# Performance work log

Measured on AMD Instinct MI355X. Metric: run time of the kernel, lower is better.

## Reference

```python
import jax, jax.numpy as jnp
import numpy as np

B, S, D, H = 4, 2048, 1024, 16
HD = D // H  # head dim = 64


def setup_inputs() -> dict:
    key = jax.random.key(0)
    ks = jax.random.split(key, 6)
    hidden_states = jax.random.normal(ks[0], (B, S, D), dtype=jnp.float32)
    attention_mask = jnp.zeros((B, S), dtype=bool)  # ignored by the module (set to None in forward)
    # RoPE cache: standard rotary angles per position
    inv_freq = 1.0 / (10000.0 ** (jnp.arange(0, HD, 2, dtype=jnp.float32) / HD))  # [HD/2]
    ang = jnp.arange(S, dtype=jnp.float32)[:, None] * inv_freq[None, :]  # [S, HD/2]
    ang = jnp.concatenate([ang, ang], axis=-1)  # [S, HD]
    rope_cos = jnp.cos(ang)
    rope_sin = jnp.sin(ang)
    scale = 1.0 / np.sqrt(D)
    Wq = jax.random.normal(ks[1], (D, D), dtype=jnp.float32) * scale
    Wk = jax.random.normal(ks[2], (D, D), dtype=jnp.float32) * scale
    Wv = jax.random.normal(ks[3], (D, D), dtype=jnp.float32) * scale
    return {"hidden_states": hidden_states, "attention_mask": attention_mask,
            "rope_cos": rope_cos, "rope_sin": rope_sin, "Wq": Wq, "Wk": Wk, "Wv": Wv}


def _rotate_half(x):
    x1, x2 = jnp.split(x, 2, axis=-1)
    return jnp.concatenate([-x2, x1], axis=-1)


def _apply_rope(x, cos, sin):
    # x: [B, H, S, HD]; cos/sin: [S, HD]
    return x * cos[None, None, :, :] + _rotate_half(x) * sin[None, None, :, :]


def reference(hidden_states, attention_mask, rope_cos, rope_sin, Wq, Wk, Wv):
    del attention_mask  # forward() sets attention_mask = None
    b, s, d = hidden_states.shape
    # QKV projections (nn.Linear: y = x @ W.T), split into heads -> [B, H, S, HD]
    def proj(W):
        y = jnp.einsum('bsd,ed->bse', hidden_states, W)
        return y.reshape(b, s, H, HD).transpose(0, 2, 1, 3)
    q = _apply_rope(proj(Wq), rope_cos, rope_sin)
    k = _apply_rope(proj(Wk), rope_cos, rope_sin)
    v = proj(Wv)
    # Softmax attention (non-causal, dropout_p=0)
    scores = jnp.einsum('bhqd,bhkd->bhqk', q, k) / np.sqrt(HD)
    probs = jax.nn.softmax(scores, axis=-1)
    ctx = jnp.einsum('bhqk,bhkd->bhqd', probs, v)
    # [B, H, S, HD] -> [B, S, D]
    return ctx.transpose(0, 2, 1, 3).reshape(b, s, d)
```

## Files before the change

### kernel.cpp

```cpp
#include <hip/hip_runtime.h>
#include <hip/hip_bf16.h>
#include <stdint.h>


typedef __attribute__((ext_vector_type(4))) float    f32x4;
typedef __attribute__((ext_vector_type(8))) __bf16   bf16x8;
typedef __attribute__((ext_vector_type(8))) unsigned short ushort8;
typedef __attribute__((ext_vector_type(4))) unsigned short ushort4v;

#define QSCALE 0.18033688011112042f
#define SMAX   16.0f

#define GLOAD_LDS16(g, l)                                                     \
  __builtin_amdgcn_global_load_lds(                                           \
      (const __attribute__((address_space(1))) void*)(g),                     \
      (__attribute__((address_space(3))) void*)(l), 16, 0, 0)

__device__ inline unsigned short bf(float f) {
  return __builtin_bit_cast(unsigned short, (__bf16)f);
}

__global__ __launch_bounds__(256) void cvt_bf16(
    const float* __restrict__ X,
    const float* __restrict__ Wq, const float* __restrict__ Wk,
    const float* __restrict__ Wv,
    unsigned short* __restrict__ Xb, unsigned short* __restrict__ Wb)
{
  const int seg = blockIdx.y;
  const float* __restrict__ src = (seg == 0) ? X : (seg == 1) ? Wq : (seg == 2) ? Wk : Wv;
  unsigned short* __restrict__ dst = (seg == 0) ? Xb : Wb + (size_t)(seg - 1) * 1048576;
  const size_t n8 = (seg == 0) ? (size_t)1048576 : (size_t)131072;
  const size_t stride = (size_t)gridDim.x * 256;
  for (size_t i = blockIdx.x * 256 + threadIdx.x; i < n8; i += stride) {
    const float4 a = *reinterpret_cast<const float4*>(src + i * 8);
    const float4 b = *reinterpret_cast<const float4*>(src + i * 8 + 4);
    ushort8 o = { bf(a.x), bf(a.y), bf(a.z), bf(a.w), bf(b.x), bf(b.y), bf(b.z), bf(b.w) };
    *reinterpret_cast<ushort8*>(dst + i * 8) = o;
  }
}

__global__ __launch_bounds__(256) void qkv_gemm(
    const unsigned short* __restrict__ Xb, const unsigned short* __restrict__ Wb,
    const float* __restrict__ rc, const float* __restrict__ rs,
    unsigned short* __restrict__ Qb, unsigned short* __restrict__ Kb,
    unsigned short* __restrict__ VbT, int col0, int nheads_c, int gx)
{
  const int nwg = gridDim.x;
  const int q8 = nwg >> 3;
  int w = (blockIdx.x % 8) * q8 + blockIdx.x / 8;
  const int z = w / (gx * 64);
  const int r = w - z * gx * 64;
  const int brow = (r / gx) * 128;
  const int bcol = (r % gx) * 128;

  const unsigned short* __restrict__ Wz = Wb + (size_t)z * 1048576;
  const bool rope = (z < 2);

  const int tid  = threadIdx.x;
  const int lane = tid & 63;
  const int wid  = tid >> 6;
  const int wm = wid >> 1, wn = wid & 1;
  const int col16 = lane & 15, rowg = lane >> 4;

  __shared__ unsigned short As[128 * 32];
  __shared__ unsigned short Bs[128 * 32];

  f32x4 acc[4][4];
  #pragma unroll
  for (int m = 0; m < 4; ++m)
    #pragma unroll
    for (int n = 0; n < 4; ++n) acc[m][n] = (f32x4)0.f;

  const int srow = wid * 16 + (lane >> 2);
  const int scol = (lane & 3) * 8;
  const unsigned short* gA0 = Xb + (size_t)(brow + srow) * 1024 + scol;
  const unsigned short* gA1 = gA0 + (size_t)64 * 1024;
  const unsigned short* gB0 = Wz + (size_t)(col0 + bcol + srow) * 1024 + scol;
  const unsigned short* gB1 = gB0 + (size_t)64 * 1024;
  unsigned short* lA0 = &As[wid * 16 * 32];
  unsigned short* lA1 = &As[(64 + wid * 16) * 32];
  unsigned short* lB0 = &Bs[wid * 16 * 32];
  unsigned short* lB1 = &Bs[(64 + wid * 16) * 32];

  for (int k0 = 0; k0 < 1024; k0 += 32) {
    GLOAD_LDS16(gA0 + k0, lA0);
    GLOAD_LDS16(gA1 + k0, lA1);
    GLOAD_LDS16(gB0 + k0, lB0);
    GLOAD_LDS16(gB1 + k0, lB1);
    __syncthreads();

    bf16x8 af[4], bfv[4];
    #pragma unroll
    for (int m = 0; m < 4; ++m)
      af[m] = __builtin_bit_cast(bf16x8, *reinterpret_cast<const ushort8*>(
                &As[(wm * 64 + m * 16 + col16) * 32 + rowg * 8]));
    #pragma unroll
    for (int n = 0; n < 4; ++n)
      bfv[n] = __builtin_bit_cast(bf16x8, *reinterpret_cast<const ushort8*>(
                &Bs[(wn * 64 + n * 16 + col16) * 32 + rowg * 8]));
    #pragma unroll
    for (int m = 0; m < 4; ++m)
      #pragma unroll
      for (int n = 0; n < 4; ++n)
        acc[m][n] = __builtin_amdgcn_mfma_f32_16x16x32_bf16(af[m], bfv[n], acc[m][n], 0, 0, 0);
    __syncthreads();
  }

  #pragma unroll
  for (int m = 0; m < 4; ++m) {
    #pragma unroll
    for (int n = 0; n < 4; ++n) {
      const int e  = bcol + wn * 64 + n * 16 + col16;
      const int hl = e >> 6, hd = e & 63;
      if (z == 2) {
        const int row0 = brow + wm * 64 + m * 16 + rowg * 4;
        const int b = row0 >> 11, s0 = row0 & 2047;
        ushort4v o = { bf(acc[m][n][0]), bf(acc[m][n][1]), bf(acc[m][n][2]), bf(acc[m][n][3]) };
        *reinterpret_cast<ushort4v*>(
            VbT + ((size_t)(b * nheads_c + hl) * 64 + hd) * 2048 + s0) = o;
      } else {
        unsigned short* __restrict__ outp = (z == 0) ? Qb : Kb;
        #pragma unroll
        for (int j = 0; j < 4; ++j) {
          const int row = brow + wm * 64 + m * 16 + rowg * 4 + j;
          const int b = row >> 11, s = row & 2047;
          const float rot = (n < 2) ? -acc[m][n + 2][j] : acc[m][n - 2][j];
          float v = acc[m][n][j] * rc[s * 64 + hd] + rot * rs[s * 64 + hd];
          if (z == 0) v *= QSCALE;
          outp[((size_t)(b * nheads_c + hl) * 2048 + s) * 64 + hd] = bf(v);
        }
      }
    }
  }
}

__global__ __launch_bounds__(256) void attn(
    const unsigned short* __restrict__ Qb, const unsigned short* __restrict__ Kb,
    const unsigned short* __restrict__ VbT, float* __restrict__ out,
    int col0, int nheads_c)
{
  const int tid = threadIdx.x, lane = tid & 63, wq = tid >> 6;
  const int col16 = lane & 15, rowg = lane >> 4;

  int wg = blockIdx.x;
  const int qx = (int)gridDim.x >> 3;
  wg = (wg & 7) * qx + (wg >> 3);
  const int bh = wg >> 4;
  const int q0 = (wg & 15) * 128;
  const int b = bh / nheads_c, hl = bh - b * nheads_c;
  const int hg = (col0 >> 6) + hl;
  const size_t base = (size_t)bh * 2048 * 64;

  __shared__ unsigned short Ks[64 * 72];
  __shared__ unsigned short Vt[64 * 72];
  __shared__ unsigned short Ps[128 * 76];

  {
    const int r = tid >> 3, c = (tid & 7) * 8;
    #pragma unroll
    for (int p = 0; p < 4; ++p) {
      const int row = p * 32 + r;
      ushort8 v = *reinterpret_cast<const ushort8*>(Qb + base + (size_t)(q0 + row) * 64 + c);
      *reinterpret_cast<ushort8*>(&Ps[row * 76 + c]) = v;
    }
  }
  __syncthreads();
  bf16x8 qf[2][2];
  #pragma unroll
  for (int m = 0; m < 2; ++m)
    #pragma unroll
    for (int ks = 0; ks < 2; ++ks)
      qf[m][ks] = __builtin_bit_cast(bf16x8, *reinterpret_cast<const ushort8*>(
          &Ps[(wq * 32 + m * 16 + col16) * 76 + ks * 32 + rowg * 8]));

  float lsum[2][4];
  f32x4 acc[2][4];
  #pragma unroll
  for (int m = 0; m < 2; ++m)
    #pragma unroll
    for (int j = 0; j < 4; ++j) lsum[m][j] = 0.f;
  #pragma unroll
  for (int m = 0; m < 2; ++m)
    #pragma unroll
    for (int hf = 0; hf < 4; ++hf) acc[m][hf] = (f32x4)0.f;

  for (int kt = 0; kt < 32; ++kt) {
    const int key0 = kt * 64;
    {
      const int r = tid >> 3, c = (tid & 7) * 8;
      #pragma unroll
      for (int p = 0; p < 2; ++p) {
        ushort8 kv = *reinterpret_cast<const ushort8*>(Kb + base + (size_t)(key0 + p * 32 + r) * 64 + c);
        *reinterpret_cast<ushort8*>(&Ks[(p * 32 + r) * 72 + c]) = kv;
      }
      const int vr = tid >> 2, vc = (tid & 3) * 16;
      ushort8 v0 = *reinterpret_cast<const ushort8*>(VbT + base + (size_t)vr * 2048 + key0 + vc);
      ushort8 v1 = *reinterpret_cast<const ushort8*>(VbT + base + (size_t)vr * 2048 + key0 + vc + 8);
      *reinterpret_cast<ushort8*>(&Vt[vr * 72 + vc]) = v0;
      *reinterpret_cast<ushort8*>(&Vt[vr * 72 + vc + 8]) = v1;
    }
    __syncthreads();

    f32x4 sc[2][4];
    #pragma unroll
    for (int m = 0; m < 2; ++m)
      #pragma unroll
      for (int kf = 0; kf < 4; ++kf) sc[m][kf] = (f32x4)0.f;
    __builtin_amdgcn_s_setprio(1);
    #pragma unroll
    for (int kf = 0; kf < 4; ++kf) {
      #pragma unroll
      for (int ks = 0; ks < 2; ++ks) {
        bf16x8 kfrag = __builtin_bit_cast(bf16x8, *reinterpret_cast<const ushort8*>(
            &Ks[(kf * 16 + col16) * 72 + ks * 32 + rowg * 8]));
        sc[0][kf] = __builtin_amdgcn_mfma_f32_16x16x32_bf16(qf[0][ks], kfrag, sc[0][kf], 0, 0, 0);
        sc[1][kf] = __builtin_amdgcn_mfma_f32_16x16x32_bf16(qf[1][ks], kfrag, sc[1][kf], 0, 0, 0);
      }
    }
    __builtin_amdgcn_s_setprio(0);

    #pragma unroll
    for (int m = 0; m < 2; ++m)
      #pragma unroll
      for (int j = 0; j < 4; ++j) {
        float ps = 0.f;
        #pragma unroll
        for (int kf = 0; kf < 4; ++kf) {
          const float p = __builtin_exp2f(sc[m][kf][j] - SMAX);
          sc[m][kf][j] = p;
          ps += p;
        }
        lsum[m][j] += ps;
      }

    #pragma unroll
    for (int m = 0; m < 2; ++m)
      #pragma unroll
      for (int kf = 0; kf < 4; ++kf)
        #pragma unroll
        for (int j = 0; j < 4; ++j)
          Ps[(wq * 32 + m * 16 + rowg * 4 + j) * 76 + kf * 16 + col16] = bf(sc[m][kf][j]);
    __syncthreads();

    __builtin_amdgcn_s_setprio(1);
    #pragma unroll
    for (int ks = 0; ks < 2; ++ks) {
      bf16x8 pf[2];
      #pragma unroll
      for (int m = 0; m < 2; ++m)
        pf[m] = __builtin_bit_cast(bf16x8, *reinterpret_cast<const ushort8*>(
            &Ps[(wq * 32 + m * 16 + col16) * 76 + ks * 32 + rowg * 8]));
      #pragma unroll
      for (int hf = 0; hf < 4; ++hf) {
        bf16x8 vf = __builtin_bit_cast(bf16x8, *reinterpret_cast<const ushort8*>(
            &Vt[(hf * 16 + col16) * 72 + ks * 32 + rowg * 8]));
        acc[0][hf] = __builtin_amdgcn_mfma_f32_16x16x32_bf16(pf[0], vf, acc[0][hf], 0, 0, 0);
        acc[1][hf] = __builtin_amdgcn_mfma_f32_16x16x32_bf16(pf[1], vf, acc[1][hf], 0, 0, 0);
      }
    }
    __builtin_amdgcn_s_setprio(0);
    __syncthreads();
  }

  #pragma unroll
  for (int m = 0; m < 2; ++m)
    #pragma unroll
    for (int j = 0; j < 4; ++j) {
      float l = lsum[m][j];
      l += __shfl_xor(l, 1);
      l += __shfl_xor(l, 2);
      l += __shfl_xor(l, 4);
      l += __shfl_xor(l, 8);
      const float inv = 1.0f / l;
      const int s = q0 + wq * 32 + m * 16 + rowg * 4 + j;
      #pragma unroll
      for (int hf = 0; hf < 4; ++hf) {
        const int hd = hf * 16 + col16;
        out[((size_t)(b * 2048 + s)) * 1024 + hg * 64 + hd] = acc[m][hf][j] * inv;
      }
    }
}

extern "C" void kernel_launch(void* const* d_in, const int* in_sizes, int n_in,
                              void* d_out, int out_size, void* d_ws, size_t ws_size,
                              hipStream_t stream) {
  (void)in_sizes; (void)n_in; (void)out_size;
  const float* X  = (const float*)d_in[0];
  const float* rc = (const float*)d_in[2];
  const float* rs = (const float*)d_in[3];
  const float* Wq = (const float*)d_in[4];
  const float* Wk = (const float*)d_in[5];
  const float* Wv = (const float*)d_in[6];
  float* out = (float*)d_out;

  const size_t fixed = (size_t)2 * 8192 * 1024 + (size_t)3 * 2 * 1024 * 1024;
  int NC = 8;
  for (int nc = 1; nc <= 8; nc <<= 1) {
    size_t need = (size_t)3 * 2 * 8192 * (1024 / nc) + fixed;
    if (need <= ws_size) { NC = nc; break; }
  }
  const int CW = 1024 / NC;
  const int nheads_c = CW >> 6;
  const int nBH = 4 * nheads_c;
  const int gx = CW / 128;
  const size_t pc = (size_t)8192 * CW;

  unsigned short* Qb  = (unsigned short*)d_ws;
  unsigned short* Kb  = Qb + pc;
  unsigned short* VbT = Kb + pc;
  unsigned short* Xb  = VbT + pc;
  unsigned short* Wb  = Xb + (size_t)8192 * 1024;

  cvt_bf16<<<dim3(512, 4), 256, 0, stream>>>(X, Wq, Wk, Wv, Xb, Wb);

  for (int c = 0; c < NC; ++c) {
    const int col0 = c * CW;
    qkv_gemm<<<dim3(gx * 64 * 3), 256, 0, stream>>>(
        Xb, Wb, rc, rs, Qb, Kb, VbT, col0, nheads_c, gx);
    attn<<<dim3(16 * nBH), 256, 0, stream>>>(
        Qb, Kb, VbT, out, col0, nheads_c);
  }
}
```

Before: 206.0 us.

## Prefetch next K/V tile into registers during attention compute

The attention loop now issues the global loads for the next 64-key K and V tile into registers before computing the current tile. After the PV MFMAs those registers are written to LDS, so global latency overlaps with compute instead of stalling at the top of each iteration. The first tile is preloaded together with Q, and the s_setprio wave-priority hints are removed. It costs extra registers per thread, which may lower occupancy.

```diff
diff --git a/kernel.cpp b/kernel.cpp
--- a/kernel.cpp
+++ b/kernel.cpp
@@ -54,7 +54,6 @@
   const int bcol = (r % gx) * 128;
 
   const unsigned short* __restrict__ Wz = Wb + (size_t)z * 1048576;
-  const bool rope = (z < 2);
 
   const int tid  = threadIdx.x;
   const int lane = tid & 63;
@@ -155,16 +154,27 @@
   __shared__ unsigned short Vt[64 * 72];
   __shared__ unsigned short Ps[128 * 76];
 
+  const int r  = tid >> 3, c  = (tid & 7) * 8;
+  const int vr = tid >> 2, vc = (tid & 3) * 16;
+
+  #pragma unroll
+  for (int p = 0; p < 4; ++p) {
+    const int row = p * 32 + r;
+    ushort8 v = *reinterpret_cast<const ushort8*>(Qb + base + (size_t)(q0 + row) * 64 + c);
+    *reinterpret_cast<ushort8*>(&Ps[row * 76 + c]) = v;
+  }
   {
-    const int r = tid >> 3, c = (tid & 7) * 8;
-    #pragma unroll
-    for (int p = 0; p < 4; ++p) {
-      const int row = p * 32 + r;
-      ushort8 v = *reinterpret_cast<const ushort8*>(Qb + base + (size_t)(q0 + row) * 64 + c);
-      *reinterpret_cast<ushort8*>(&Ps[row * 76 + c]) = v;
-    }
+    ushort8 k0 = *reinterpret_cast<const ushort8*>(Kb + base + (size_t)r * 64 + c);
+    ushort8 k1 = *reinterpret_cast<const ushort8*>(Kb + base + (size_t)(32 + r) * 64 + c);
+    ushort8 v0 = *reinterpret_cast<const ushort8*>(VbT + base + (size_t)vr * 2048 + vc);
+    ushort8 v1 = *reinterpret_cast<const ushort8*>(VbT + base + (size_t)vr * 2048 + vc + 8);
+    *reinterpret_cast<ushort8*>(&Ks[r * 72 + c]) = k0;
+    *reinterpret_cast<ushort8*>(&Ks[(32 + r) * 72 + c]) = k1;
+    *reinterpret_cast<ushort8*>(&Vt[vr * 72 + vc]) = v0;
+    *reinterpret_cast<ushort8*>(&Vt[vr * 72 + vc + 8]) = v1;
   }
   __syncthreads();
+
   bf16x8 qf[2][2];
   #pragma unroll
   for (int m = 0; m < 2; ++m)
@@ -185,28 +195,20 @@
     for (int hf = 0; hf < 4; ++hf) acc[m][hf] = (f32x4)0.f;
 
   for (int kt = 0; kt < 32; ++kt) {
-    const int key0 = kt * 64;
-    {
-      const int r = tid >> 3, c = (tid & 7) * 8;
-      #pragma unroll
-      for (int p = 0; p < 2; ++p) {
-        ushort8 kv = *reinterpret_cast<const ushort8*>(Kb + base + (size_t)(key0 + p * 32 + r) * 64 + c);
-        *reinterpret_cast<ushort8*>(&Ks[(p * 32 + r) * 72 + c]) = kv;
-      }
-      const int vr = tid >> 2, vc = (tid & 3) * 16;
-      ushort8 v0 = *reinterpret_cast<const ushort8*>(VbT + base + (size_t)vr * 2048 + key0 + vc);
-      ushort8 v1 = *reinterpret_cast<const ushort8*>(VbT + base + (size_t)vr * 2048 + key0 + vc + 8);
-      *reinterpret_cast<ushort8*>(&Vt[vr * 72 + vc]) = v0;
-      *reinterpret_cast<ushort8*>(&Vt[vr * 72 + vc + 8]) = v1;
-    }
-    __syncthreads();
+    ushort8 nk0, nk1, nv0, nv1;
+    if (kt < 31) {
+      const int kn = (kt + 1) * 64;
+      nk0 = *reinterpret_cast<const ushort8*>(Kb + base + (size_t)(kn + r) * 64 + c);
+      nk1 = *reinterpret_cast<const ushort8*>(Kb + base + (size_t)(kn + 32 + r) * 64 + c);
+      nv0 = *reinterpret_cast<const ushort8*>(VbT + base + (size_t)vr * 2048 + kn + vc);
+      nv1 = *reinterpret_cast<const ushort8*>(VbT + base + (size_t)vr * 2048 + kn + vc + 8);
+    }
 
     f32x4 sc[2][4];
     #pragma unroll
     for (int m = 0; m < 2; ++m)
       #pragma unroll
       for (int kf = 0; kf < 4; ++kf) sc[m][kf] = (f32x4)0.f;
-    __builtin_amdgcn_s_setprio(1);
     #pragma unroll
     for (int kf = 0; kf < 4; ++kf) {
       #pragma unroll
@@ -217,7 +219,6 @@
         sc[1][kf] = __builtin_amdgcn_mfma_f32_16x16x32_bf16(qf[1][ks], kfrag, sc[1][kf], 0, 0, 0);
       }
     }
-    __builtin_amdgcn_s_setprio(0);
 
     #pragma unroll
     for (int m = 0; m < 2; ++m)
@@ -242,7 +243,6 @@
           Ps[(wq * 32 + m * 16 + rowg * 4 + j) * 76 + kf * 16 + col16] = bf(sc[m][kf][j]);
     __syncthreads();
 
-    __builtin_amdgcn_s_setprio(1);
     #pragma unroll
     for (int ks = 0; ks < 2; ++ks) {
       bf16x8 pf[2];
@@ -258,8 +258,15 @@
         acc[1][hf] = __builtin_amdgcn_mfma_f32_16x16x32_bf16(pf[1], vf, acc[1][hf], 0, 0, 0);
       }
     }
-    __builtin_amdgcn_s_setprio(0);
     __syncthreads();
+
+    if (kt < 31) {
+      *reinterpret_cast<ushort8*>(&Ks[r * 72 + c]) = nk0;
+      *reinterpret_cast<ushort8*>(&Ks[(32 + r) * 72 + c]) = nk1;
+      *reinterpret_cast<ushort8*>(&Vt[vr * 72 + vc]) = nv0;
+      *reinterpret_cast<ushort8*>(&Vt[vr * 72 + vc + 8]) = nv1;
+      __syncthreads();
+    }
   }
 
   #pragma unroll
```

After: 216.7 us. +5.2%, slower.

## Double-buffer K/V tiles via direct-to-LDS loads with XOR swizzle and MFMA row sums

Applied to the files above, without the earlier changes.

The attention kernel now prefetches the next K and V^T tiles straight into a second LDS buffer using global_load_lds, so global loads overlap the current tile's compute. Those tiles use an unpadded, XOR-swizzled layout to avoid bank conflicts. The softmax denominator is now computed by an extra MFMA against a ones matrix, replacing the per-lane exp sums and the shuffle reduction. It also drops the s_setprio hints and the barrier between the P writes and P reads, relying on each wave touching only its own Ps rows. The risk is synchronization: nothing explicitly waits for the async prefetch to land apart from the end-of-iteration barrier, and there is extra LDS use and extra MFMA work.

```diff
diff --git a/kernel.cpp b/kernel.cpp
--- a/kernel.cpp
+++ b/kernel.cpp
@@ -11,7 +11,7 @@
 #define QSCALE 0.18033688011112042f
 #define SMAX   16.0f
 
-#define GLOAD_LDS16(g, l)                                                     \
+#define GL16(g, l)                                                            \
   __builtin_amdgcn_global_load_lds(                                           \
       (const __attribute__((address_space(1))) void*)(g),                     \
       (__attribute__((address_space(3))) void*)(l), 16, 0, 0)
@@ -54,7 +54,6 @@
   const int bcol = (r % gx) * 128;
 
   const unsigned short* __restrict__ Wz = Wb + (size_t)z * 1048576;
-  const bool rope = (z < 2);
 
   const int tid  = threadIdx.x;
   const int lane = tid & 63;
@@ -83,10 +82,10 @@
   unsigned short* lB1 = &Bs[(64 + wid * 16) * 32];
 
   for (int k0 = 0; k0 < 1024; k0 += 32) {
-    GLOAD_LDS16(gA0 + k0, lA0);
-    GLOAD_LDS16(gA1 + k0, lA1);
-    GLOAD_LDS16(gB0 + k0, lB0);
-    GLOAD_LDS16(gB1 + k0, lB1);
+    GL16(gA0 + k0, lA0);
+    GL16(gA1 + k0, lA1);
+    GL16(gB0 + k0, lB0);
+    GL16(gB1 + k0, lB1);
     __syncthreads();
 
     bf16x8 af[4], bfv[4];
@@ -151,87 +150,84 @@
   const int hg = (col0 >> 6) + hl;
   const size_t base = (size_t)bh * 2048 * 64;
 
-  __shared__ unsigned short Ks[64 * 72];
-  __shared__ unsigned short Vt[64 * 72];
-  __shared__ unsigned short Ps[128 * 76];
-
+  __shared__ unsigned short Ks[2][64 * 64];
+  __shared__ unsigned short Vt[2][64 * 64];
+  __shared__ unsigned short Ps[128 * 68];
+  __shared__ unsigned short Ones[16 * 64];
+
+  const int sr = lane >> 3, ch = lane & 7;
+
+  {
+    const int row = tid >> 4, c4 = (tid & 15) * 4;
+    const unsigned short v = (row == 0) ? (unsigned short)0x3F80 : (unsigned short)0;
+    ushort4v o = { v, v, v, v };
+    *reinterpret_cast<ushort4v*>(&Ones[row * 64 + c4]) = o;
+  }
+
+  #pragma unroll
+  for (int p = 0; p < 2; ++p) {
+    const int rr = wq * 16 + p * 8 + sr;
+    GL16(Kb + base + (size_t)rr * 64 + ((ch ^ sr) << 3), &Ks[0][(wq * 16 + p * 8) * 64]);
+    GL16(VbT + base + (size_t)rr * 2048 + ((ch ^ sr) << 3), &Vt[0][(wq * 16 + p * 8) * 64]);
+  }
   {
     const int r = tid >> 3, c = (tid & 7) * 8;
     #pragma unroll
     for (int p = 0; p < 4; ++p) {
       const int row = p * 32 + r;
       ushort8 v = *reinterpret_cast<const ushort8*>(Qb + base + (size_t)(q0 + row) * 64 + c);
-      *reinterpret_cast<ushort8*>(&Ps[row * 76 + c]) = v;
+      *reinterpret_cast<ushort8*>(&Ps[row * 68 + c]) = v;
     }
   }
   __syncthreads();
+
   bf16x8 qf[2][2];
   #pragma unroll
   for (int m = 0; m < 2; ++m)
     #pragma unroll
     for (int ks = 0; ks < 2; ++ks)
       qf[m][ks] = __builtin_bit_cast(bf16x8, *reinterpret_cast<const ushort8*>(
-          &Ps[(wq * 32 + m * 16 + col16) * 76 + ks * 32 + rowg * 8]));
-
-  float lsum[2][4];
-  f32x4 acc[2][4];
-  #pragma unroll
-  for (int m = 0; m < 2; ++m)
-    #pragma unroll
-    for (int j = 0; j < 4; ++j) lsum[m][j] = 0.f;
-  #pragma unroll
-  for (int m = 0; m < 2; ++m)
+          &Ps[(wq * 32 + m * 16 + col16) * 68 + ks * 32 + rowg * 8]));
+
+  f32x4 acc[2][4], accL[2];
+  #pragma unroll
+  for (int m = 0; m < 2; ++m) {
+    accL[m] = (f32x4)0.f;
     #pragma unroll
     for (int hf = 0; hf < 4; ++hf) acc[m][hf] = (f32x4)0.f;
-
+  }
+
+  const int swz = col16 & 7;
+
+  int cur = 0;
   for (int kt = 0; kt < 32; ++kt) {
-    const int key0 = kt * 64;
-    {
-      const int r = tid >> 3, c = (tid & 7) * 8;
+    if (kt < 31) {
+      const int kn = (kt + 1) * 64;
       #pragma unroll
       for (int p = 0; p < 2; ++p) {
-        ushort8 kv = *reinterpret_cast<const ushort8*>(Kb + base + (size_t)(key0 + p * 32 + r) * 64 + c);
-        *reinterpret_cast<ushort8*>(&Ks[(p * 32 + r) * 72 + c]) = kv;
-      }
-      const int vr = tid >> 2, vc = (tid & 3) * 16;
-      ushort8 v0 = *reinterpret_cast<const ushort8*>(VbT + base + (size_t)vr * 2048 + key0 + vc);
-      ushort8 v1 = *reinterpret_cast<const ushort8*>(VbT + base + (size_t)vr * 2048 + key0 + vc + 8);
-      *reinterpret_cast<ushort8*>(&Vt[vr * 72 + vc]) = v0;
-      *reinterpret_cast<ushort8*>(&Vt[vr * 72 + vc + 8]) = v1;
-    }
-    __syncthreads();
+        const int rr = wq * 16 + p * 8 + sr;
+        GL16(Kb + base + (size_t)(kn + rr) * 64 + ((ch ^ sr) << 3),
+             &Ks[cur ^ 1][(wq * 16 + p * 8) * 64]);
+        GL16(VbT + base + (size_t)rr * 2048 + kn + ((ch ^ sr) << 3),
+             &Vt[cur ^ 1][(wq * 16 + p * 8) * 64]);
+      }
+    }
 
     f32x4 sc[2][4];
     #pragma unroll
     for (int m = 0; m < 2; ++m)
       #pragma unroll
       for (int kf = 0; kf < 4; ++kf) sc[m][kf] = (f32x4)0.f;
-    __builtin_amdgcn_s_setprio(1);
     #pragma unroll
     for (int kf = 0; kf < 4; ++kf) {
       #pragma unroll
       for (int ks = 0; ks < 2; ++ks) {
         bf16x8 kfrag = __builtin_bit_cast(bf16x8, *reinterpret_cast<const ushort8*>(
-            &Ks[(kf * 16 + col16) * 72 + ks * 32 + rowg * 8]));
+            &Ks[cur][(kf * 16 + col16) * 64 + (((4 * ks + rowg) ^ swz) << 3)]));
         sc[0][kf] = __builtin_amdgcn_mfma_f32_16x16x32_bf16(qf[0][ks], kfrag, sc[0][kf], 0, 0, 0);
         sc[1][kf] = __builtin_amdgcn_mfma_f32_16x16x32_bf16(qf[1][ks], kfrag, sc[1][kf], 0, 0, 0);
       }
     }
-    __builtin_amdgcn_s_setprio(0);
-
-    #pragma unroll
-    for (int m = 0; m < 2; ++m)
-      #pragma unroll
-      for (int j = 0; j < 4; ++j) {
-        float ps = 0.f;
-        #pragma unroll
-        for (int kf = 0; kf < 4; ++kf) {
-          const float p = __builtin_exp2f(sc[m][kf][j] - SMAX);
-          sc[m][kf][j] = p;
-          ps += p;
-        }
-        lsum[m][j] += ps;
-      }
 
     #pragma unroll
     for (int m = 0; m < 2; ++m)
@@ -239,38 +235,37 @@
       for (int kf = 0; kf < 4; ++kf)
         #pragma unroll
         for (int j = 0; j < 4; ++j)
-          Ps[(wq * 32 + m * 16 + rowg * 4 + j) * 76 + kf * 16 + col16] = bf(sc[m][kf][j]);
-    __syncthreads();
-
-    __builtin_amdgcn_s_setprio(1);
+          Ps[(wq * 32 + m * 16 + rowg * 4 + j) * 68 + kf * 16 + col16] =
+              bf(__builtin_exp2f(sc[m][kf][j] - SMAX));
+
     #pragma unroll
     for (int ks = 0; ks < 2; ++ks) {
       bf16x8 pf[2];
       #pragma unroll
       for (int m = 0; m < 2; ++m)
         pf[m] = __builtin_bit_cast(bf16x8, *reinterpret_cast<const ushort8*>(
-            &Ps[(wq * 32 + m * 16 + col16) * 76 + ks * 32 + rowg * 8]));
+            &Ps[(wq * 32 + m * 16 + col16) * 68 + ks * 32 + rowg * 8]));
       #pragma unroll
       for (int hf = 0; hf < 4; ++hf) {
         bf16x8 vf = __builtin_bit_cast(bf16x8, *reinterpret_cast<const ushort8*>(
-            &Vt[(hf * 16 + col16) * 72 + ks * 32 + rowg * 8]));
+            &Vt[cur][(hf * 16 + col16) * 64 + (((4 * ks + rowg) ^ swz) << 3)]));
         acc[0][hf] = __builtin_amdgcn_mfma_f32_16x16x32_bf16(pf[0], vf, acc[0][hf], 0, 0, 0);
         acc[1][hf] = __builtin_amdgcn_mfma_f32_16x16x32_bf16(pf[1], vf, acc[1][hf], 0, 0, 0);
       }
-    }
-    __builtin_amdgcn_s_setprio(0);
+      bf16x8 of = __builtin_bit_cast(bf16x8, *reinterpret_cast<const ushort8*>(
+          &Ones[col16 * 64 + ks * 32 + rowg * 8]));
+      accL[0] = __builtin_amdgcn_mfma_f32_16x16x32_bf16(pf[0], of, accL[0], 0, 0, 0);
+      accL[1] = __builtin_amdgcn_mfma_f32_16x16x32_bf16(pf[1], of, accL[1], 0, 0, 0);
+    }
     __syncthreads();
+    cur ^= 1;
   }
 
   #pragma unroll
   for (int m = 0; m < 2; ++m)
     #pragma unroll
     for (int j = 0; j < 4; ++j) {
-      float l = lsum[m][j];
-      l += __shfl_xor(l, 1);
-      l += __shfl_xor(l, 2);
-      l += __shfl_xor(l, 4);
-      l += __shfl_xor(l, 8);
+      const float l = __shfl(accL[m][j], lane & 48);
       const float inv = 1.0f / l;
       const int s = q0 + wq * 32 + m * 16 + rowg * 4 + j;
       #pragma unroll
```

Result: slower. 224.8 us (+9.1%).
